# Performance work log

Hardware: AMD Instinct MI355X
Metric: run time of the kernel (lower is better)

## Reference

```python
import jax, jax.numpy as jnp
import numpy as np

N_NODES = 100000
N_EDGES = 6400000
D_FEAT = 128
HIDDEN = 16


def _gcn_conv(x, row, col, W, b, n):
    # PyG GCNConv: add self-loops, symmetric norm, message from row -> aggregated at col
    h = x @ W  # [N, out]
    loop = jnp.arange(n, dtype=row.dtype)
    r = jnp.concatenate([row, loop])
    c = jnp.concatenate([col, loop])
    ones = jnp.ones(r.shape[0], dtype=x.dtype)
    deg = jax.ops.segment_sum(ones, c, num_segments=n)  # in-degree incl. self-loop
    dinv = jnp.where(deg > 0, jax.lax.rsqrt(deg), 0.0)
    norm = dinv[r] * dinv[c]  # [E+N]
    msg = h[r] * norm[:, None]  # [E+N, out]
    out = jax.ops.segment_sum(msg, c, num_segments=n)
    return out + b


def setup_inputs() -> dict:
    key = jax.random.key(0)
    ks = jax.random.split(key, 8)
    x = jax.random.normal(ks[0], (N_NODES, D_FEAT), dtype=jnp.float32)
    edge_attr = jax.random.normal(ks[1], (N_EDGES, 1), dtype=jnp.float32)
    edge_row = jnp.sort(jax.random.randint(ks[2], (N_EDGES,), 0, N_NODES, dtype=jnp.int32)).astype(jnp.int64)
    edge_col = jax.random.randint(ks[3], (N_EDGES,), 0, N_NODES, dtype=jnp.int32).astype(jnp.int64)
    W1 = jax.random.normal(ks[4], (D_FEAT + 1, HIDDEN), dtype=jnp.float32) * (1.0 / np.sqrt(D_FEAT + 1))
    b1 = jnp.zeros((HIDDEN,), dtype=jnp.float32)
    W2 = jax.random.normal(ks[5], (HIDDEN, 1), dtype=jnp.float32) * (1.0 / np.sqrt(HIDDEN))
    b2 = jnp.zeros((1,), dtype=jnp.float32)
    return {"x": x, "edge_attr": edge_attr, "edge_row": edge_row, "edge_col": edge_col,
            "W1": W1, "b1": b1, "W2": W2, "b2": b2}


def reference(x, edge_attr, edge_row, edge_col, W1, b1, W2, b2):
    n = x.shape[0]
    # the original Python loop == segment-sum of edge_attr by source node (rows are sorted)
    x_edge = jax.ops.segment_sum(edge_attr, edge_row, num_segments=n)  # [N, 1]
    h = jnp.concatenate([x, x_edge], axis=1)  # [N, D+1]
    h = _gcn_conv(h, edge_row, edge_col, W1, b1, n)
    h = jax.nn.relu(h)
    # dropout is identity in eval mode
    out = _gcn_conv(h, edge_row, edge_col, W2, b2, n)  # [N, 1]
    return out
```

## Files before the change

kernel.cpp:

```cpp
#include <hip/hip_runtime.h>


#define D_FEAT 128
#define HIDDEN 16
#define TILE 8192
#define CAP 17408u
#define FXS 262144.0f
#define FXSI 3.814697265625e-06f

__device__ inline float bf2f(unsigned short u) {
    union { unsigned x; float f; } t; t.x = ((unsigned)u) << 16; return t.f;
}

__global__ __launch_bounds__(256) void k_init(float* xe, unsigned* gcur, int n, int nb) {
    int t = blockIdx.x * 256 + threadIdx.x;
    if (t < n) xe[t] = 0.f;
    if (t < nb) gcur[t * 16] = (unsigned)t * CAP;
}

__global__ __launch_bounds__(1024) void k_sortplace(const int* __restrict__ row,
                                                    const int* __restrict__ col,
                                                    const float* __restrict__ ea,
                                                    float* __restrict__ xe,
                                                    unsigned* __restrict__ gcur,
                                                    unsigned* __restrict__ ebufP,
                                                    int ne, int nb) {
    __shared__ unsigned stage[TILE];
    __shared__ unsigned short sbuck[TILE];
    __shared__ unsigned h[512], base_[512], cursor[512], gb_[512];
    __shared__ unsigned wsum[8];
    int tid = threadIdx.x;
    int lane = tid & 63;
    int w = tid >> 6;
    int tile0 = blockIdx.x * TILE;
    int cnt_t = min(TILE, ne - tile0);
    if (tid < 512) h[tid] = 0u;
    __syncthreads();
    int rr[8], cc[8];
    float aa[8];
    #pragma unroll
    for (int k = 0; k < 8; ++k) {
        int e = tile0 + tid + k * 1024;
        if (e < ne) {
            rr[k] = row[e]; cc[k] = col[e]; aa[k] = ea[e];
            atomicAdd(&h[cc[k] >> 8], 1u);
        } else { rr[k] = -1; cc[k] = 0; aa[k] = 0.f; }
    }
    #pragma unroll
    for (int k = 0; k < 8; ++k) {
        int r = rr[k];
        float a = aa[k];
        #pragma unroll
        for (int d = 1; d < 64; d <<= 1) {
            float up = __shfl_up(a, d);
            int  rup = __shfl_up(r, d);
            if (lane >= d && rup == r) a += up;
        }
        int rdn = __shfl_down(r, 1);
        bool tail = (lane == 63) || (rdn != r);
        if (r >= 0 && tail) unsafeAtomicAdd(&xe[r], a);
    }
    __syncthreads();
    unsigned hv = 0, s = 0;
    if (tid < 512) {
        hv = h[tid];
        s = hv;
        #pragma unroll
        for (int d = 1; d < 64; d <<= 1) {
            unsigned u = __shfl_up(s, d);
            if (lane >= d) s += u;
        }
        if (lane == 63) wsum[w] = s;
    }
    __syncthreads();
    if (tid < 512) {
        unsigned woff = 0;
        #pragma unroll
        for (int i = 0; i < 8; ++i) woff += (i < w) ? wsum[i] : 0u;
        unsigned ex = s + woff - hv;
        base_[tid] = ex;
        cursor[tid] = ex;
        if (tid < nb && hv) gb_[tid] = atomicAdd(&gcur[tid * 16], hv);
    }
    __syncthreads();
    #pragma unroll
    for (int k = 0; k < 8; ++k) {
        if (rr[k] >= 0) {
            int b = cc[k] >> 8;
            unsigned p = atomicAdd(&cursor[b], 1u);
            stage[p] = (((unsigned)(cc[k] & 255)) << 24) | (unsigned)rr[k];
            sbuck[p] = (unsigned short)b;
        }
    }
    __syncthreads();
    for (int t = tid; t < cnt_t; t += 1024) {
        unsigned b = sbuck[t];
        unsigned pos = gb_[b] + ((unsigned)t - base_[b]);
        if (pos < (b + 1u) * CAP) ebufP[pos] = stage[t];
    }
}

__global__ __launch_bounds__(512) void k_deghist(const unsigned* __restrict__ gcur,
                                                 const unsigned* __restrict__ ebufP,
                                                 unsigned* __restrict__ deg,
                                                 unsigned* __restrict__ stG, int n) {
    __shared__ unsigned dg[256];
    __shared__ unsigned wsum[4];
    int tid = threadIdx.x, b = blockIdx.x, lane = tid & 63;
    if (tid < 256) dg[tid] = 0u;
    __syncthreads();
    unsigned base = (unsigned)b * CAP;
    unsigned m = min(gcur[b * 16] - base, CAP);
    unsigned i = tid;
    for (; i + 1536 < m; i += 2048) {
        unsigned pk0 = ebufP[base + i];
        unsigned pk1 = ebufP[base + i + 512];
        unsigned pk2 = ebufP[base + i + 1024];
        unsigned pk3 = ebufP[base + i + 1536];
        atomicAdd(&dg[pk0 >> 24], 1u);
        atomicAdd(&dg[pk1 >> 24], 1u);
        atomicAdd(&dg[pk2 >> 24], 1u);
        atomicAdd(&dg[pk3 >> 24], 1u);
    }
    for (; i < m; i += 512) atomicAdd(&dg[ebufP[base + i] >> 24], 1u);
    __syncthreads();
    unsigned dval = 0, s = 0;
    if (tid < 256) {
        dval = dg[tid];
        s = dval;
        #pragma unroll
        for (int d = 1; d < 64; d <<= 1) {
            unsigned uu = __shfl_up(s, d);
            if (lane >= d) s += uu;
        }
        if (lane == 63) wsum[tid >> 6] = s;
    }
    __syncthreads();
    if (tid < 256) {
        int w = tid >> 6;
        unsigned woff = 0;
        #pragma unroll
        for (int i2 = 0; i2 < 4; ++i2) woff += (i2 < w) ? wsum[i2] : 0u;
        unsigned ex = s + woff - dval;
        int v = b * 256 + tid;
        if (v < n) { deg[v] = dval; stG[v] = base + ex; }
    }
}

__global__ __launch_bounds__(256) void k_gemm1(const float* __restrict__ x,
                                               const float* __restrict__ xe,
                                               const unsigned* __restrict__ deg,
                                               const float* __restrict__ W1,
                                               float* __restrict__ g,
                                               unsigned short* __restrict__ gb, int n) {
    __shared__ float WsT[16 * 132];
    __shared__ float xs[64 * 132];
    int tid = threadIdx.x;
    for (int idx = tid; idx < 129 * 16; idx += 256) {
        int k = idx >> 4, j = idx & 15;
        WsT[j * 132 + k] = W1[idx];
    }
    int n0 = blockIdx.x * 64;
    const float4* x4 = (const float4*)x;
    for (int idx = tid; idx < 64 * 32; idx += 256) {
        int r = idx >> 5, c = idx & 31;
        float4 v = (n0 + r < n) ? x4[(size_t)(n0 + r) * 32 + c]
                                : make_float4(0.f, 0.f, 0.f, 0.f);
        *(float4*)&xs[r * 132 + c * 4] = v;
    }
    if (tid < 64) {
        int r = tid;
        xs[r * 132 + 128] = (n0 + r < n) ? xe[n0 + r] : 0.f;
    }
    __syncthreads();
    int j  = tid & 15;
    int nb = tid >> 4;
    const float* wrow = &WsT[j * 132];
    for (int rep = 0; rep < 4; ++rep) {
        int nl = nb + (rep << 4);
        int node = n0 + nl;
        const float* xrow = &xs[nl * 132];
        float acc = 0.f;
        #pragma unroll
        for (int k = 0; k < 128; k += 4) {
            float4 xv = *(const float4*)&xrow[k];
            float4 wv = *(const float4*)&wrow[k];
            acc += xv.x * wv.x;
            acc += xv.y * wv.y;
            acc += xv.z * wv.z;
            acc += xv.w * wv.w;
        }
        acc += xrow[128] * wrow[128];
        if (node < n) {
            float v = acc * rsqrtf((float)deg[node] + 1.0f);
            g[(size_t)node * 16 + j] = v;
            union { float f; unsigned u; } cv; cv.f = v;
            unsigned r16 = (cv.u + 0x7FFFu + ((cv.u >> 16) & 1u)) >> 16;
            gb[(size_t)node * 16 + j] = (unsigned short)r16;
        }
    }
}

__global__ __launch_bounds__(512) void k_agg1s(const unsigned* __restrict__ gcur,
                                               const unsigned* __restrict__ ebufP,
                                               const unsigned* __restrict__ deg,
                                               const unsigned* __restrict__ stG,
                                               const unsigned* __restrict__ gu,
                                               const float* __restrict__ g,
                                               const float* __restrict__ b1,
                                               const float* __restrict__ W2,
                                               float* __restrict__ g2, int n) {
    __shared__ unsigned sorted[CAP];
    __shared__ unsigned dg[256], st[256], cur[256];
    int tid = threadIdx.x, b = blockIdx.x;
    unsigned base = (unsigned)b * CAP;
    unsigned m = min(gcur[b * 16] - base, CAP);
    if (tid < 256) {
        int v = b * 256 + tid;
        unsigned dval = (v < n) ? deg[v] : 0u;
        unsigned sv   = (v < n) ? stG[v] - base : 0u;
        dg[tid] = dval;
        st[tid] = sv;
        cur[tid] = sv;
    }
    __syncthreads();
    unsigned i = tid;
    for (; i + 1536 < m; i += 2048) {
        unsigned pk0 = ebufP[base + i];
        unsigned pk1 = ebufP[base + i + 512];
        unsigned pk2 = ebufP[base + i + 1024];
        unsigned pk3 = ebufP[base + i + 1536];
        unsigned p0 = atomicAdd(&cur[pk0 >> 24], 1u);
        unsigned p1 = atomicAdd(&cur[pk1 >> 24], 1u);
        unsigned p2 = atomicAdd(&cur[pk2 >> 24], 1u);
        unsigned p3 = atomicAdd(&cur[pk3 >> 24], 1u);
        if (p0 < CAP) sorted[p0] = pk0 & 0xFFFFFFu;
        if (p1 < CAP) sorted[p1] = pk1 & 0xFFFFFFu;
        if (p2 < CAP) sorted[p2] = pk2 & 0xFFFFFFu;
        if (p3 < CAP) sorted[p3] = pk3 & 0xFFFFFFu;
    }
    for (; i < m; i += 512) {
        unsigned pk = ebufP[base + i];
        unsigned p = atomicAdd(&cur[pk >> 24], 1u);
        if (p < CAP) sorted[p] = pk & 0xFFFFFFu;
    }
    __syncthreads();
    const uint4* gu4 = (const uint4*)gu;
    int grp = tid >> 4;
    int u = tid & 1;
    int oct = (tid >> 1) & 7;
    float4 bbA = ((const float4*)b1)[2 * u];
    float4 bbB = ((const float4*)b1)[2 * u + 1];
    float4 wwA = ((const float4*)W2)[2 * u];
    float4 wwB = ((const float4*)W2)[2 * u + 1];
    for (int it = 0; it < 8; ++it) {
        int c = it * 32 + grp;
        int v = b * 256 + c;
        if (v >= n) break;
        unsigned s0 = st[c], e0 = s0 + dg[c];
        float a0 = 0.f, a1 = 0.f, a2 = 0.f, a3 = 0.f;
        float a4 = 0.f, a5 = 0.f, a6 = 0.f, a7 = 0.f;
        float c0 = 0.f, c1 = 0.f, c2 = 0.f, c3 = 0.f;
        float c4 = 0.f, c5 = 0.f, c6 = 0.f, c7 = 0.f;
        unsigned q = s0 + oct;
        for (; q + 8 < e0; q += 16) {
            uint4 w0 = gu4[(size_t)sorted[q] * 2 + u];
            uint4 w1 = gu4[(size_t)sorted[q + 8] * 2 + u];
            a0 += bf2f((unsigned short)w0.x); a1 += bf2f((unsigned short)(w0.x >> 16));
            a2 += bf2f((unsigned short)w0.y); a3 += bf2f((unsigned short)(w0.y >> 16));
            a4 += bf2f((unsigned short)w0.z); a5 += bf2f((unsigned short)(w0.z >> 16));
            a6 += bf2f((unsigned short)w0.w); a7 += bf2f((unsigned short)(w0.w >> 16));
            c0 += bf2f((unsigned short)w1.x); c1 += bf2f((unsigned short)(w1.x >> 16));
            c2 += bf2f((unsigned short)w1.y); c3 += bf2f((unsigned short)(w1.y >> 16));
            c4 += bf2f((unsigned short)w1.z); c5 += bf2f((unsigned short)(w1.z >> 16));
            c6 += bf2f((unsigned short)w1.w); c7 += bf2f((unsigned short)(w1.w >> 16));
        }
        for (; q < e0; q += 8) {
            uint4 w0 = gu4[(size_t)sorted[q] * 2 + u];
            a0 += bf2f((unsigned short)w0.x); a1 += bf2f((unsigned short)(w0.x >> 16));
            a2 += bf2f((unsigned short)w0.y); a3 += bf2f((unsigned short)(w0.y >> 16));
            a4 += bf2f((unsigned short)w0.z); a5 += bf2f((unsigned short)(w0.z >> 16));
            a6 += bf2f((unsigned short)w0.w); a7 += bf2f((unsigned short)(w0.w >> 16));
        }
        a0 += c0; a1 += c1; a2 += c2; a3 += c3;
        a4 += c4; a5 += c5; a6 += c6; a7 += c7;
        #pragma unroll
        for (int d = 2; d <= 8; d <<= 1) {
            a0 += __shfl_xor(a0, d, 16);
            a1 += __shfl_xor(a1, d, 16);
            a2 += __shfl_xor(a2, d, 16);
            a3 += __shfl_xor(a3, d, 16);
            a4 += __shfl_xor(a4, d, 16);
            a5 += __shfl_xor(a5, d, 16);
            a6 += __shfl_xor(a6, d, 16);
            a7 += __shfl_xor(a7, d, 16);
        }
        float di = rsqrtf((float)dg[c] + 1.0f);
        float4 gA = ((const float4*)g)[(size_t)v * 4 + 2 * u];
        float4 gB = ((const float4*)g)[(size_t)v * 4 + 2 * u + 1];
        float v0 = fmaxf(di * (gA.x + a0) + bbA.x, 0.f);
        float v1 = fmaxf(di * (gA.y + a1) + bbA.y, 0.f);
        float v2 = fmaxf(di * (gA.z + a2) + bbA.z, 0.f);
        float v3 = fmaxf(di * (gA.w + a3) + bbA.w, 0.f);
        float v4 = fmaxf(di * (gB.x + a4) + bbB.x, 0.f);
        float v5 = fmaxf(di * (gB.y + a5) + bbB.y, 0.f);
        float v6 = fmaxf(di * (gB.z + a6) + bbB.z, 0.f);
        float v7 = fmaxf(di * (gB.w + a7) + bbB.w, 0.f);
        float prd = v0 * wwA.x + v1 * wwA.y + v2 * wwA.z + v3 * wwA.w
                  + v4 * wwB.x + v5 * wwB.y + v6 * wwB.z + v7 * wwB.w;
        prd += __shfl_xor(prd, 1, 16);
        if ((tid & 15) == 0) g2[v] = prd * di;
    }
}

__global__ __launch_bounds__(512) void k_agg2i(const unsigned* __restrict__ gcur,
                                               const unsigned* __restrict__ ebufP,
                                               const unsigned* __restrict__ deg,
                                               const float* __restrict__ g2,
                                               const float* __restrict__ b2,
                                               float* __restrict__ out, int n) {
    __shared__ int acc2[256];
    int tid = threadIdx.x, b = blockIdx.x;
    if (tid < 256) acc2[tid] = 0;
    __syncthreads();
    unsigned base = (unsigned)b * CAP;
    unsigned m = min(gcur[b * 16] - base, CAP);
    unsigned mt = m & ~3u;
    const uint4* eb4 = (const uint4*)(ebufP + base);
    for (unsigned t = tid; t * 4 + 3 < m; t += 512) {
        uint4 pk = eb4[t];
        float v0 = g2[pk.x & 0xFFFFFFu];
        float v1 = g2[pk.y & 0xFFFFFFu];
        float v2 = g2[pk.z & 0xFFFFFFu];
        float v3 = g2[pk.w & 0xFFFFFFu];
        atomicAdd(&acc2[pk.x >> 24], __float2int_rn(v0 * FXS));
        atomicAdd(&acc2[pk.y >> 24], __float2int_rn(v1 * FXS));
        atomicAdd(&acc2[pk.z >> 24], __float2int_rn(v2 * FXS));
        atomicAdd(&acc2[pk.w >> 24], __float2int_rn(v3 * FXS));
    }
    for (unsigned t = mt + tid; t < m; t += 512) {
        unsigned pk = ebufP[base + t];
        atomicAdd(&acc2[pk >> 24], __float2int_rn(g2[pk & 0xFFFFFFu] * FXS));
    }
    __syncthreads();
    if (tid < 256) {
        int v = b * 256 + tid;
        if (v < n) {
            float a = (float)acc2[tid] * FXSI;
            float di = rsqrtf((float)deg[v] + 1.0f);
            out[v] = di * (g2[v] + a) + b2[0];
        }
    }
}

extern "C" void kernel_launch(void* const* d_in, const int* in_sizes, int n_in,
                              void* d_out, int out_size, void* d_ws, size_t ws_size,
                              hipStream_t stream) {
    const float* x   = (const float*)d_in[0];
    const float* ea  = (const float*)d_in[1];
    const int*   row = (const int*)d_in[2];
    const int*   col = (const int*)d_in[3];
    const float* W1  = (const float*)d_in[4];
    const float* b1  = (const float*)d_in[5];
    const float* W2  = (const float*)d_in[6];
    const float* b2  = (const float*)d_in[7];
    float* out = (float*)d_out;

    int n  = in_sizes[0] / D_FEAT;
    int ne = in_sizes[2];
    int nb = (n + 255) >> 8;

    float* ws   = (float*)d_ws;
    float* xe   = ws;
    float* g    = ws + (size_t)n;
    float* g2   = ws + (size_t)17 * n;
    unsigned short* gbuf = (unsigned short*)(ws + (size_t)18 * n);
    unsigned* deg  = (unsigned*)(ws + (size_t)26 * n);
    unsigned* stG  = deg + (size_t)n;
    unsigned* gcur = stG + (size_t)n;
    unsigned* ebufP = gcur + (size_t)nb * 16;

    dim3 blk(256);
    int g_node = (n + 255) / 256;
    int g_tile = (ne + TILE - 1) / TILE;
    int g_gemm = (n + 63) / 64;

    k_init<<<g_node, blk, 0, stream>>>(xe, gcur, n, nb);
    k_sortplace<<<g_tile, 1024, 0, stream>>>(row, col, ea, xe, gcur, ebufP, ne, nb);
    k_deghist<<<nb, 512, 0, stream>>>(gcur, ebufP, deg, stG, n);
    k_gemm1<<<g_gemm, blk, 0, stream>>>(x, xe, deg, W1, g, gbuf, n);
    k_agg1s<<<nb, 512, 0, stream>>>(gcur, ebufP, deg, stG, (const unsigned*)gbuf, g, b1, W2, g2, n);
    k_agg2i<<<nb, 512, 0, stream>>>(gcur, ebufP, deg, g2, b2, out, n);
}
```

Before: 271.0 us.

## Vectorize edge loads per thread and replace per-element segmented scans with one chained scan

Each thread now loads 8 consecutive edges with int4/float4 vector loads instead of 8 strided scalar loads. The segmented sum over sorted rows is done serially within each thread, followed by a single cross-lane segmented scan that carries partial sums between threads, in place of eight separate 6-step shuffle scans. This cuts shuffle work and global atomics on xe, at the cost of more complex boundary logic. Stage order within a tile changes, though downstream placement stays consistent.

Result: faster. 257.0 us (-5.2%).

```diff
diff --git a/kernel.cpp b/kernel.cpp
--- a/kernel.cpp
+++ b/kernel.cpp
@@ -36,48 +36,85 @@
     int cnt_t = min(TILE, ne - tile0);
     if (tid < 512) h[tid] = 0u;
     __syncthreads();
+    int e0 = tile0 + tid * 8;
     int rr[8], cc[8];
     float aa[8];
+    if (e0 + 7 < ne) {
+        int4 r0 = *(const int4*)&row[e0];
+        int4 r1 = *(const int4*)&row[e0 + 4];
+        int4 c0 = *(const int4*)&col[e0];
+        int4 c1 = *(const int4*)&col[e0 + 4];
+        float4 a0 = *(const float4*)&ea[e0];
+        float4 a1 = *(const float4*)&ea[e0 + 4];
+        rr[0] = r0.x; rr[1] = r0.y; rr[2] = r0.z; rr[3] = r0.w;
+        rr[4] = r1.x; rr[5] = r1.y; rr[6] = r1.z; rr[7] = r1.w;
+        cc[0] = c0.x; cc[1] = c0.y; cc[2] = c0.z; cc[3] = c0.w;
+        cc[4] = c1.x; cc[5] = c1.y; cc[6] = c1.z; cc[7] = c1.w;
+        aa[0] = a0.x; aa[1] = a0.y; aa[2] = a0.z; aa[3] = a0.w;
+        aa[4] = a1.x; aa[5] = a1.y; aa[6] = a1.z; aa[7] = a1.w;
+    } else {
+        #pragma unroll
+        for (int k = 0; k < 8; ++k) {
+            int e = e0 + k;
+            if (e < ne) { rr[k] = row[e]; cc[k] = col[e]; aa[k] = ea[e]; }
+            else        { rr[k] = -1; cc[k] = 0; aa[k] = 0.f; }
+        }
+    }
     #pragma unroll
-    for (int k = 0; k < 8; ++k) {
-        int e = tile0 + tid + k * 1024;
-        if (e < ne) {
-            rr[k] = row[e]; cc[k] = col[e]; aa[k] = ea[e];
-            atomicAdd(&h[cc[k] >> 8], 1u);
-        } else { rr[k] = -1; cc[k] = 0; aa[k] = 0.f; }
-    }
+    for (int k = 0; k < 8; ++k)
+        if (rr[k] >= 0) atomicAdd(&h[cc[k] >> 8], 1u);
+    int r_first = rr[0];
+    float run = aa[0], lead = 0.f;
     #pragma unroll
-    for (int k = 0; k < 8; ++k) {
-        int r = rr[k];
-        float a = aa[k];
-        #pragma unroll
-        for (int d = 1; d < 64; d <<= 1) {
-            float up = __shfl_up(a, d);
-            int  rup = __shfl_up(r, d);
-            if (lane >= d && rup == r) a += up;
-        }
-        int rdn = __shfl_down(r, 1);
-        bool tail = (lane == 63) || (rdn != r);
-        if (r >= 0 && tail) unsafeAtomicAdd(&xe[r], a);
-    }
-    __syncthreads();
-    unsigned hv = 0, s = 0;
+    for (int k = 1; k < 8; ++k) {
+        if (rr[k] == rr[k - 1]) run += aa[k];
+        else {
+            if (rr[k - 1] == r_first) lead = run;
+            else if (rr[k - 1] >= 0) unsafeAtomicAdd(&xe[rr[k - 1]], run);
+            run = aa[k];
+        }
+    }
+    int r_last = rr[7];
+    float trail = run;
+    bool puref = (r_first == r_last);
+    int rl_prev = __shfl_up(r_last, 1);
+    bool m = (lane > 0) && (r_first == rl_prev);
+    float s = trail;
+    int f = (puref && m) ? 0 : 1;
+    #pragma unroll
+    for (int d = 1; d < 64; d <<= 1) {
+        float su = __shfl_up(s, d);
+        int fu = __shfl_up(f, d);
+        if (lane >= d) {
+            if (!f) s += su;
+            f = f | fu;
+        }
+    }
+    float o_prev = __shfl_up(s, 1);
+    float inflow = m ? o_prev : 0.f;
+    int rf_next = __shfl_down(r_first, 1);
+    bool chain_end = (lane == 63) || (rf_next != r_last);
+    if (!puref && r_first >= 0) unsafeAtomicAdd(&xe[r_first], lead + inflow);
+    if (chain_end && r_last >= 0)
+        unsafeAtomicAdd(&xe[r_last], trail + (puref ? inflow : 0.f));
+    __syncthreads();
+    unsigned hv = 0, sh = 0;
     if (tid < 512) {
         hv = h[tid];
-        s = hv;
+        sh = hv;
         #pragma unroll
         for (int d = 1; d < 64; d <<= 1) {
-            unsigned u = __shfl_up(s, d);
-            if (lane >= d) s += u;
-        }
-        if (lane == 63) wsum[w] = s;
+            unsigned u = __shfl_up(sh, d);
+            if (lane >= d) sh += u;
+        }
+        if (lane == 63) wsum[w] = sh;
     }
     __syncthreads();
     if (tid < 512) {
         unsigned woff = 0;
         #pragma unroll
         for (int i = 0; i < 8; ++i) woff += (i < w) ? wsum[i] : 0u;
-        unsigned ex = s + woff - hv;
+        unsigned ex = sh + woff - hv;
         base_[tid] = ex;
         cursor[tid] = ex;
         if (tid < nb && hv) gb_[tid] = atomicAdd(&gcur[tid * 16], hv);
```
